# Kernel tuning notes

Hardware: AMD Instinct MI355X
Metric: run time of the kernel (lower is better)

Reference implementation:

```python
import jax, jax.numpy as jnp
import numpy as np

B, N, K = 8, 1024, 20


def _w(key, o, i):
    return jax.random.normal(key, (o, i), dtype=jnp.float32) * (1.0 / np.sqrt(i))


def setup_inputs() -> dict:
    key = jax.random.key(0)
    ks = iter(jax.random.split(key, 64))
    d = {"inputs": jax.random.normal(next(ks), (B, 3, N, 1), dtype=jnp.float32)}
    shapes = {
        "he_w1": (32, 12), "he_w2": (64, 32), "hn_w1": (32, 67), "hn_w2": (64, 32),
        "b1e_w1": (48, 192), "b1e_w2": (128, 48), "b1n_w1": (48, 192), "b1n_w2": (128, 48),
        "b2e_w1": (96, 384), "b2e_w2": (192, 96), "b2n_w1": (96, 320), "b2n_w2": (192, 96),
        "f_w": (512, 384), "p1_w": (256, 512), "p2_w": (128, 256), "p3_w": (40, 128),
    }
    for name, (o, i) in shapes.items():
        d[name] = _w(next(ks), o, i)
        d[name.replace("_w", "_b")] = jnp.zeros((o,), dtype=jnp.float32)
    return d


def _conv(x, w, b):
    # BasicConv with norm=None: 1x1 Conv2d + bias. x: [B,C,N,k]
    return jnp.einsum('bcnk,oc->bonk', x, w) + b[None, :, None, None]


def _conv_relu(x, w, b):
    return jax.nn.relu(_conv(x, w, b))


def _gather(x, idx):
    # batched_index_select: x [B,C,N,1], idx [B,N,k] -> [B,C,N,k]
    b, c, n, _ = x.shape
    k = idx.shape[-1]
    out = jnp.take_along_axis(x[:, :, :, 0], idx.reshape(b, 1, n * k), axis=2)
    return out.reshape(b, c, n, k)


def _knn(x, k):
    # DenseKnnGraph: x [B,C,N,1] -> (nn_idx, center_idx), each [B,N,k]
    xt = jnp.transpose(x[:, :, :, 0], (0, 2, 1))  # [B,N,C]
    sq = jnp.sum(xt * xt, axis=-1, keepdims=True)
    dist = sq - 2.0 * jnp.einsum('bnc,bmc->bnm', xt, xt) + jnp.transpose(sq, (0, 2, 1))
    _, nn_idx = jax.lax.top_k(-dist, k)
    center = jnp.broadcast_to(jnp.arange(x.shape[2])[None, :, None], nn_idx.shape)
    return nn_idx, center


def _mp(nf, e_ij, nn_idx, center, ew1, eb1, ew2, eb2, nw1, nb1, nw2, nb2):
    # MessagePassing block (Kearnes et al. style)
    h_i = _gather(nf, center)  # [B,Cin,N,k]
    h_j = _gather(nf, nn_idx)
    e_p = _conv_relu(_conv_relu(jnp.concatenate([e_ij, h_i, h_j], axis=1), ew1, eb1), ew2, eb2)
    m = jnp.broadcast_to(jnp.sum(e_p, axis=3, keepdims=True),
                         e_p.shape[:3] + (h_i.shape[-1],))
    h_p = _conv_relu(_conv_relu(jnp.concatenate([h_i, m], axis=1), nw1, nb1), nw2, nb2)
    return h_p[:, :, :, 0:1], e_p


def reference(inputs, he_w1, he_b1, he_w2, he_b2, hn_w1, hn_b1, hn_w2, hn_b2,
              b1e_w1, b1e_b1, b1e_w2, b1e_b2, b1n_w1, b1n_b1, b1n_w2, b1n_b2,
              b2e_w1, b2e_b1, b2e_w2, b2e_b2, b2n_w1, b2n_b1, b2n_w2, b2n_b2,
              f_w, f_b, p1_w, p1_b, p2_w, p2_b, p3_w, p3_b):
    nn_idx, center = _knn(inputs[:, 0:3], K)
    # initial edge features: (h_i, h_i - h_j) on xyz-KNN graph
    gh_i = _gather(inputs, center)
    gh_j = _gather(inputs, nn_idx)
    e_ij = jnp.concatenate([gh_i, gh_i - gh_j], axis=1)  # [B, 2*in, N, k]
    h1, e1 = _mp(inputs, e_ij, nn_idx, center, he_w1, he_b1, he_w2, he_b2, hn_w1, hn_b1, hn_w2, hn_b2)
    h2, e2 = _mp(h1, e1, nn_idx, center, b1e_w1, b1e_b1, b1e_w2, b1e_b2, b1n_w1, b1n_b1, b1n_w2, b1n_b2)
    h3, e3 = _mp(h2, e2, nn_idx, center, b2e_w1, b2e_b1, b2e_w2, b2e_b2, b2n_w1, b2n_b1, b2n_w2, b2n_b2)
    feats = jnp.concatenate([h1, h2, h3], axis=1)  # [B, 384, N, 1]
    fus = _conv_relu(feats, f_w, f_b)  # [B, 512, N, 1]
    pooled = jnp.max(fus, axis=(2, 3), keepdims=True)  # max_pool2d over [N,1]
    # prediction head (dropout = identity at inference)
    pred = _conv(_conv_relu(_conv_relu(pooled, p1_w, p1_b), p2_w, p2_b), p3_w, p3_b)
    return pred[:, :, :, 0], inputs  # (logits [B,n_classes,1], edge_features)
```

## Files before the change

kernel.cpp:

```cpp
#include <hip/hip_runtime.h>

#define BDIM 8
#define NDIM 1024
#define KNN 20

typedef unsigned short u16;
typedef float f32x4 __attribute__((ext_vector_type(4)));
typedef short short8 __attribute__((ext_vector_type(8)));
typedef unsigned short ushort8 __attribute__((ext_vector_type(8)));

__device__ inline u16 f2bf(float f) {
  unsigned u = __float_as_uint(f);
  unsigned r = (u + 0x7fffu + ((u >> 16) & 1u)) >> 16;
  return (u16)r;
}
__device__ inline float bf2f(u16 v) {
  return __uint_as_float(((unsigned)v) << 16);
}

__global__ __launch_bounds__(256) void knn_wcvt(
    const float* __restrict__ x, int* __restrict__ nn,
    const float* __restrict__ w1_3, const float* __restrict__ w2_3,
    const float* __restrict__ w1_2, const float* __restrict__ w2_2,
    const float* __restrict__ hn_w1, const float* __restrict__ f_w,
    const float* __restrict__ he_w1, const float* __restrict__ he_w2,
    const float* __restrict__ bn_w1, const float* __restrict__ bn_w2,
    u16* __restrict__ w1b3e, u16* __restrict__ wpq3, u16* __restrict__ w2b3,
    u16* __restrict__ w1b2e, u16* __restrict__ wpq2, u16* __restrict__ w2b2,
    float* __restrict__ w1p1, u16* __restrict__ fwb,
    u16* __restrict__ w1b1, u16* __restrict__ w2b1,
    u16* __restrict__ wn1b, u16* __restrict__ wn2b, int* __restrict__ pooled) {
  const int tid = threadIdx.x;
  if (blockIdx.x >= BDIM * 256) {
    const int idx = (blockIdx.x - BDIM * 256) * 256 + tid;
    if (idx < 512 * 384) fwb[idx] = f2bf(f_w[idx]);
    if (idx < 96 * 128) {
      int oc = idx >> 7, c = idx & 127;
      w1b3e[idx] = f2bf(w1_3[oc * 384 + c]);
    }
    if (idx < 192 * 128) {
      int n = idx >> 7, c = idx & 127;
      wpq3[idx] = f2bf(n < 96 ? w1_3[n * 384 + 128 + c]
                              : w1_3[(n - 96) * 384 + 256 + c]);
    }
    if (idx < 192 * 96) w2b3[idx] = f2bf(w2_3[idx]);
    if (idx < 48 * 64) {
      int oc = idx >> 6, c = idx & 63;
      w1b2e[idx] = f2bf(w1_2[oc * 192 + c]);
    }
    if (idx < 96 * 64) {
      int n = idx >> 6, c = idx & 63;
      wpq2[idx] = f2bf(n < 48 ? w1_2[n * 192 + 64 + c]
                              : w1_2[(n - 48) * 192 + 128 + c]);
    }
    if (idx < 128 * 64) {
      int oc = idx >> 6, i = idx & 63;
      w2b2[idx] = (i < 48) ? f2bf(w2_2[oc * 48 + i]) : (u16)0;
    }
    if (idx < 32 * 68) {
      int oc = idx / 68, c = idx - oc * 68;
      w1p1[idx] = (c < 67) ? hn_w1[oc * 67 + c] : 0.0f;
    }
    if (idx < 32 * 32) {
      int oc = idx >> 5, c = idx & 31;
      w1b1[idx] = (c < 12) ? f2bf(he_w1[oc * 12 + c]) : (u16)0;
    }
    if (idx < 64 * 32) w2b1[idx] = f2bf(he_w2[idx]);
    if (idx < 96 * 320) wn1b[idx] = f2bf(bn_w1[idx]);
    if (idx < 192 * 96) wn2b[idx] = f2bf(bn_w2[idx]);
    if (idx < BDIM * 512) pooled[idx] = 0;
    return;
  }
  {
#pragma clang fp contract(off)
    __shared__ float xs0[NDIM], xs1[NDIM], xs2[NDIM], sq[NDIM];
    const int lane = tid & 63;
    const int w = tid >> 6;
    const int b = blockIdx.x >> 8;
    const int n = ((blockIdx.x & 255) << 2) + w;
    for (int i = tid; i < NDIM; i += 256) {
      float a0 = x[(b * 3 + 0) * NDIM + i];
      float a1 = x[(b * 3 + 1) * NDIM + i];
      float a2 = x[(b * 3 + 2) * NDIM + i];
      xs0[i] = a0; xs1[i] = a1; xs2[i] = a2;
      sq[i] = (a0 * a0 + a1 * a1) + a2 * a2;
    }
    __syncthreads();
    const float xn0 = xs0[n], xn1 = xs1[n], xn2 = xs2[n], sqn = sq[n];
    float dl[16];
#pragma unroll
    for (int t = 0; t < 16; ++t) {
      int m = t * 64 + lane;
      float dot = (xn0 * xs0[m] + xn1 * xs1[m]) + xn2 * xs2[m];
      dl[t] = (sqn - 2.0f * dot) + sq[m];
    }
    int* nnrow = &nn[(b * NDIM + n) * KNN];
    for (int r = 0; r < KNN; ++r) {
      float bd = dl[0];
      int bt = 0;
#pragma unroll
      for (int t = 1; t < 16; ++t) {
        if (dl[t] < bd) { bd = dl[t]; bt = t; }
      }
      int bi = bt * 64 + lane;
#pragma unroll
      for (int off = 1; off < 64; off <<= 1) {
        float pd = __shfl_xor(bd, off);
        int pi = __shfl_xor(bi, off);
        if (pd < bd || (pd == bd && pi < bi)) { bd = pd; bi = pi; }
      }
      if (lane == 0) nnrow[r] = bi;
      if ((bi & 63) == lane) {
        int wt = bi >> 6;
#pragma unroll
        for (int t = 0; t < 16; ++t) {
          if (t == wt) dl[t] = 3.4e38f;
        }
      }
    }
  }
}

template <int PTS, int CE, int CMID, int COUT, bool WRITE_E, bool FIRST>
__global__ __launch_bounds__(256) void edge_mfma(
    const u16* __restrict__ eprev, const float* __restrict__ finput,
    const int* __restrict__ nnb, const u16* __restrict__ w1b,
    const float* __restrict__ b1v, const u16* __restrict__ w2b,
    const float* __restrict__ b2v, const u16* __restrict__ pq,
    u16* __restrict__ eout, float* __restrict__ mout) {
  constexpr int K2 = (CMID + 31) & ~31;
  constexpr int NPQ = 2 * CMID;
  constexpr int MT = PTS * KNN;
  constexpr int MTL = MT / 16;
  constexpr int XPB = CE + 8;
  constexpr int QYP = K2 + 8;
  __shared__ u16 Xs[MT * XPB];
  __shared__ u16 QY[MT * QYP];
  __shared__ float pld[FIRST ? 8 : PTS * CMID];
  const int tid = threadIdx.x;
  const int lane = tid & 63;
  const int wv = tid >> 6;
  const int q = lane >> 4;
  const int bn0 = blockIdx.x * PTS;
  const int b = bn0 >> 10;
  if constexpr (FIRST) {
    for (int idx = tid; idx < MT * (CE / 8); idx += 256) {
      int p = idx / (CE / 8), kc = idx - p * (CE / 8);
      int k0 = kc * 8;
      int bn = bn0 + p / KNN;
      int n = bn & (NDIM - 1);
      int j = nnb[(size_t)bn0 * KNN + p];
      ushort8 r;
#pragma unroll
      for (int t = 0; t < 8; ++t) {
        int c = k0 + t;
        float v = 0.0f;
        if (c < 3) v = finput[(b * 3 + c) * NDIM + n];
        else if (c < 6)
          v = finput[(b * 3 + c - 3) * NDIM + n] -
              finput[(b * 3 + c - 3) * NDIM + j];
        else if (c < 9) v = finput[(b * 3 + c - 6) * NDIM + n];
        else if (c < 12) v = finput[(b * 3 + c - 9) * NDIM + j];
        r[t] = f2bf(v);
      }
      *(ushort8*)&Xs[p * XPB + k0] = r;
    }
  } else {
    constexpr int KC = CE / 8;
    for (int ch = tid; ch < MT * KC; ch += 256) {
      int p = ch / KC, kc = ch - p * KC;
      int k0 = kc * 8;
      *(uint4*)&Xs[p * XPB + k0] =
          *(const uint4*)&eprev[((size_t)blockIdx.x * MT + p) * CE + k0];
    }
    constexpr int QC = CMID / 8;
    for (int i = tid; i < MT * QC; i += 256) {
      int p = i / QC, c8 = (i - p * QC) * 8;
      int j = nnb[(size_t)bn0 * KNN + p];
      *(uint4*)&QY[p * QYP + c8] =
          *(const uint4*)&pq[((size_t)(b << 10) + j) * NPQ + CMID + c8];
    }
    if constexpr (K2 != CMID) {
      constexpr int PC = (K2 - CMID) / 8;
      for (int i = tid; i < MT * PC; i += 256) {
        int p = i / PC, c8 = CMID + (i - p * PC) * 8;
        uint4 z = {0, 0, 0, 0};
        *(uint4*)&QY[p * QYP + c8] = z;
      }
    }
    for (int i = tid; i < PTS * CMID; i += 256) {
      int pt = i / CMID, c = i - pt * CMID;
      pld[i] = bf2f(pq[(size_t)(bn0 + pt) * NPQ + c]) + b1v[c];
    }
  }
  __syncthreads();
  {
    constexpr int NT1 = CMID / 16;
    constexpr int J1 = MTL * NT1;
    constexpr int KS1 = CE / 32;
    for (int job = wv; job < J1; job += 4) {
      int mt = job / NT1, nt = job - mt * NT1;
      int row = mt * 16 + (lane & 15);
      int ncol = nt * 16 + (lane & 15);
      int kb = q * 8;
      f32x4 acc = {0.f, 0.f, 0.f, 0.f};
      const u16* ap = &Xs[row * XPB + kb];
      const u16* bp = &w1b[(size_t)ncol * CE + kb];
#pragma unroll
      for (int ks = 0; ks < KS1; ++ks) {
        short8 a = *(const short8*)(ap + ks * 32);
        short8 bb = *(const short8*)(bp + ks * 32);
        acc = __builtin_amdgcn_mfma_f32_16x16x32_bf16(a, bb, acc, 0, 0, 0);
      }
      int m0 = mt * 16 + q * 4;
      if constexpr (FIRST) {
        float bias = b1v[ncol];
#pragma unroll
        for (int r = 0; r < 4; ++r) {
          float yv = fmaxf(acc[r] + bias, 0.0f);
          QY[(m0 + r) * QYP + ncol] = f2bf(yv);
        }
      } else {
        int pt = m0 / KNN;
        float padd = pld[pt * CMID + ncol];
#pragma unroll
        for (int r = 0; r < 4; ++r) {
          int m = m0 + r;
          float qadd = bf2f(QY[m * QYP + ncol]);
          float yv = fmaxf(acc[r] + padd + qadd, 0.0f);
          QY[m * QYP + ncol] = f2bf(yv);
        }
      }
    }
  }
  __syncthreads();
  {
    constexpr int NT2 = COUT / 16;
    constexpr int KS2 = K2 / 32;
    for (int nt = wv; nt < NT2; nt += 4) {
      int ncol = nt * 16 + (lane & 15);
      int kb = q * 8;
      short8 bfrag[KS2];
      const u16* bp = &w2b[(size_t)ncol * K2 + kb];
#pragma unroll
      for (int ks = 0; ks < KS2; ++ks)
        bfrag[ks] = *(const short8*)(bp + ks * 32);
      float bias = b2v[ncol];
      float s[PTS];
#pragma unroll
      for (int pt = 0; pt < PTS; ++pt) s[pt] = 0.0f;
#pragma unroll
      for (int mt = 0; mt < MTL; ++mt) {
        f32x4 acc = {0.f, 0.f, 0.f, 0.f};
        const u16* ap = &QY[(mt * 16 + (lane & 15)) * QYP + kb];
#pragma unroll
        for (int ks = 0; ks < KS2; ++ks) {
          short8 a = *(const short8*)(ap + ks * 32);
          acc = __builtin_amdgcn_mfma_f32_16x16x32_bf16(a, bfrag[ks], acc, 0, 0, 0);
        }
        int m0 = mt * 16 + q * 4;
        float part = 0.0f;
#pragma unroll
        for (int r = 0; r < 4; ++r) {
          float yv = fmaxf(acc[r] + bias, 0.0f);
          if (WRITE_E)
            eout[((size_t)blockIdx.x * MT + m0 + r) * COUT + ncol] = f2bf(yv);
          part += yv;
        }
        int ptA = (4 * mt) / 5;
        int ptB = (4 * mt + 3) / 5;
        int qb = 5 * ptB - 4 * mt;
#pragma unroll
        for (int pt2 = 0; pt2 < PTS; ++pt2) {
          if (pt2 == ptA && ptA == ptB) s[pt2] += part;
          else if (pt2 == ptA) s[pt2] += (q < qb) ? part : 0.0f;
          else if (pt2 == ptB) s[pt2] += (q < qb) ? 0.0f : part;
        }
      }
#pragma unroll
      for (int pt = 0; pt < PTS; ++pt) {
        float sv = s[pt];
        sv += __shfl_xor(sv, 16);
        sv += __shfl_xor(sv, 32);
        if (lane < 16)
          mout[(size_t)(bn0 + pt) * COUT + nt * 16 + lane] = sv;
      }
    }
  }
}

template <int TP, int CH, int CM, int CINP, int CMID, int COUT, int NPQ, bool FIRSTH>
__global__ __launch_bounds__(256) void node_conv(
    const float* __restrict__ h, const float* __restrict__ inputs,
    const float* __restrict__ mbuf, const float* __restrict__ w1p,
    const float* __restrict__ b1v, const float* __restrict__ w2,
    const float* __restrict__ b2v, float* __restrict__ hout,
    const u16* __restrict__ wpq, u16* __restrict__ pq) {
  constexpr int CIN = CH + CM;
  constexpr int XP = CINP + 4;
  constexpr int Y1P = CMID + 4;
  constexpr int PG = TP / 4;
  constexpr int HP = COUT + 8;
  __shared__ float Xs[TP * XP];
  __shared__ float Y1s[TP * Y1P];
  __shared__ u16 Hb[(NPQ > 0) ? TP * HP : 8];
  const int tid = threadIdx.x;
  const int bn0 = blockIdx.x * TP;
  if constexpr (FIRSTH) {
    for (int idx = tid; idx < TP * CIN; idx += 256) {
      int p = idx / CIN, c = idx - p * CIN;
      int bn = bn0 + p;
      int b = bn >> 10, n = bn & (NDIM - 1);
      Xs[p * XP + c] = (c < CH) ? inputs[(b * 3 + c) * NDIM + n]
                                : mbuf[(size_t)bn * CM + (c - CH)];
    }
    if constexpr (CINP > CIN) {
      constexpr int PAD = CINP - CIN;
      for (int idx = tid; idx < TP * PAD; idx += 256) {
        int p = idx / PAD, c = CIN + idx % PAD;
        Xs[p * XP + c] = 0.0f;
      }
    }
  } else {
    constexpr int C4 = CIN / 4;
    for (int idx = tid; idx < TP * C4; idx += 256) {
      int p = idx / C4, c = (idx - p * C4) * 4;
      int bn = bn0 + p;
      float4 v = (c < CH) ? *(const float4*)&h[(size_t)bn * CH + c]
                          : *(const float4*)&mbuf[(size_t)bn * CM + (c - CH)];
      *(float4*)&Xs[p * XP + c] = v;
    }
  }
  __syncthreads();
  {
    constexpr int NT1 = PG * (CMID / 4);
    for (int t = tid; t < NT1; t += 256) {
      int pg = t % PG, og = t / PG;
      float acc[4][4];
#pragma unroll
      for (int j = 0; j < 4; ++j) {
        float bj = b1v[og * 4 + j];
#pragma unroll
        for (int i = 0; i < 4; ++i) acc[i][j] = bj;
      }
      for (int cin = 0; cin < CINP; cin += 4) {
        float4 xr[4], wr[4];
#pragma unroll
        for (int i = 0; i < 4; ++i)
          xr[i] = *(const float4*)&Xs[(pg * 4 + i) * XP + cin];
#pragma unroll
        for (int j = 0; j < 4; ++j)
          wr[j] = *(const float4*)&w1p[(size_t)(og * 4 + j) * CINP + cin];
#pragma unroll
        for (int i = 0; i < 4; ++i)
#pragma unroll
          for (int j = 0; j < 4; ++j) {
            acc[i][j] += xr[i].x * wr[j].x;
            acc[i][j] += xr[i].y * wr[j].y;
            acc[i][j] += xr[i].z * wr[j].z;
            acc[i][j] += xr[i].w * wr[j].w;
          }
      }
#pragma unroll
      for (int i = 0; i < 4; ++i)
#pragma unroll
        for (int j = 0; j < 4; ++j)
          Y1s[(pg * 4 + i) * Y1P + og * 4 + j] = fmaxf(acc[i][j], 0.0f);
    }
  }
  __syncthreads();
  {
    constexpr int NT2 = PG * (COUT / 4);
    for (int t = tid; t < NT2; t += 256) {
      int pg = t % PG, og = t / PG;
      float acc[4][4];
#pragma unroll
      for (int j = 0; j < 4; ++j) {
        float bj = b2v[og * 4 + j];
#pragma unroll
        for (int i = 0; i < 4; ++i) acc[i][j] = bj;
      }
      for (int cin = 0; cin < CMID; cin += 4) {
        float4 xr[4], wr[4];
#pragma unroll
        for (int i = 0; i < 4; ++i)
          xr[i] = *(const float4*)&Y1s[(pg * 4 + i) * Y1P + cin];
#pragma unroll
        for (int j = 0; j < 4; ++j)
          wr[j] = *(const float4*)&w2[(size_t)(og * 4 + j) * CMID + cin];
#pragma unroll
        for (int i = 0; i < 4; ++i)
#pragma unroll
          for (int j = 0; j < 4; ++j) {
            acc[i][j] += xr[i].x * wr[j].x;
            acc[i][j] += xr[i].y * wr[j].y;
            acc[i][j] += xr[i].z * wr[j].z;
            acc[i][j] += xr[i].w * wr[j].w;
          }
      }
#pragma unroll
      for (int i = 0; i < 4; ++i) {
        int bn = bn0 + pg * 4 + i;
#pragma unroll
        for (int j = 0; j < 4; ++j) {
          float v = fmaxf(acc[i][j], 0.0f);
          hout[(size_t)bn * COUT + og * 4 + j] = v;
          if constexpr (NPQ > 0) Hb[(pg * 4 + i) * HP + og * 4 + j] = f2bf(v);
        }
      }
    }
  }
  if constexpr (NPQ > 0) {
    __syncthreads();
    const int lane = tid & 63;
    const int wv = tid >> 6;
    constexpr int NT = NPQ / 16;
    constexpr int JOBS = (TP / 16) * NT;
    constexpr int KS = COUT / 32;
    for (int job = wv; job < JOBS; job += 4) {
      int mt = job / NT, nt = job - mt * NT;
      int row = mt * 16 + (lane & 15);
      int ncol = nt * 16 + (lane & 15);
      int kb = (lane >> 4) * 8;
      f32x4 acc = {0.f, 0.f, 0.f, 0.f};
      const u16* ap = &Hb[row * HP + kb];
      const u16* bp = &wpq[(size_t)ncol * COUT + kb];
#pragma unroll
      for (int ks = 0; ks < KS; ++ks) {
        short8 a = *(const short8*)(ap + ks * 32);
        short8 bb = *(const short8*)(bp + ks * 32);
        acc = __builtin_amdgcn_mfma_f32_16x16x32_bf16(a, bb, acc, 0, 0, 0);
      }
      int m0 = mt * 16 + (lane >> 4) * 4;
#pragma unroll
      for (int r = 0; r < 4; ++r)
        pq[(size_t)(bn0 + m0 + r) * NPQ + ncol] = f2bf(acc[r]);
    }
  }
}

__global__ __launch_bounds__(256) void fuse_pool_mfma(
    const float* __restrict__ h1, const float* __restrict__ h2,
    const float* __restrict__ m3, const u16* __restrict__ wn1b,
    const float* __restrict__ bn1v, const u16* __restrict__ wn2b,
    const float* __restrict__ bn2v, const u16* __restrict__ fwb,
    const float* __restrict__ fb, int* __restrict__ pooled) {
  constexpr int TP = 32;
  constexpr int XNP = 328;
  constexpr int Y1NP = 104;
  constexpr int XPB = 392;
  __shared__ __align__(16) char smem[TP * XPB * 2];
  u16* Xs = (u16*)smem;
  u16* Xn = (u16*)smem;
  __shared__ u16 Y1n[TP * Y1NP];
  __shared__ int pmax[512];
  const int tid = threadIdx.x;
  const int lane = tid & 63;
  const int wv = tid >> 6;
  const int q = lane >> 4;
  const int bn0 = blockIdx.x * TP;
  const int b = bn0 >> 10;
  for (int i = tid; i < 512; i += 256) pmax[i] = 0;
  for (int i = tid; i < TP * 41; i += 256) {
    int p = i / 41, kc = i - p * 41;
    int k0 = kc * 8;
    ushort8 r;
    if (kc < 16) {
      const float* src = &h2[(size_t)(bn0 + p) * 128 + k0];
      float4 f0 = *(const float4*)src;
      float4 f1 = *(const float4*)(src + 4);
      r[0] = f2bf(f0.x); r[1] = f2bf(f0.y); r[2] = f2bf(f0.z); r[3] = f2bf(f0.w);
      r[4] = f2bf(f1.x); r[5] = f2bf(f1.y); r[6] = f2bf(f1.z); r[7] = f2bf(f1.w);
    } else if (kc < 40) {
      const float* src = &m3[(size_t)(bn0 + p) * 192 + (k0 - 128)];
      float4 f0 = *(const float4*)src;
      float4 f1 = *(const float4*)(src + 4);
      r[0] = f2bf(f0.x); r[1] = f2bf(f0.y); r[2] = f2bf(f0.z); r[3] = f2bf(f0.w);
      r[4] = f2bf(f1.x); r[5] = f2bf(f1.y); r[6] = f2bf(f1.z); r[7] = f2bf(f1.w);
    } else {
#pragma unroll
      for (int t = 0; t < 8; ++t) r[t] = 0;
    }
    *(ushort8*)&Xn[p * XNP + k0] = r;
  }
  __syncthreads();
  for (int job = wv; job < 12; job += 4) {
    int mt = job / 6, nt = job - mt * 6;
    int row = mt * 16 + (lane & 15);
    int ncol = nt * 16 + (lane & 15);
    int kb = q * 8;
    f32x4 acc = {0.f, 0.f, 0.f, 0.f};
    const u16* ap = &Xn[row * XNP + kb];
    const u16* bp = &wn1b[(size_t)ncol * 320 + kb];
#pragma unroll
    for (int ks = 0; ks < 10; ++ks) {
      short8 a = *(const short8*)(ap + ks * 32);
      short8 bb = *(const short8*)(bp + ks * 32);
      acc = __builtin_amdgcn_mfma_f32_16x16x32_bf16(a, bb, acc, 0, 0, 0);
    }
    float bias = bn1v[ncol];
    int m0 = mt * 16 + q * 4;
#pragma unroll
    for (int r = 0; r < 4; ++r)
      Y1n[(m0 + r) * Y1NP + ncol] = f2bf(fmaxf(acc[r] + bias, 0.0f));
  }
  __syncthreads();
  for (int i = tid; i < TP * 24; i += 256) {
    int p = i / 24, kc = i - p * 24;
    int k0 = kc * 8;
    const float* src = (k0 < 64) ? &h1[(size_t)(bn0 + p) * 64 + k0]
                                 : &h2[(size_t)(bn0 + p) * 128 + (k0 - 64)];
    float4 f0 = *(const float4*)src;
    float4 f1 = *(const float4*)(src + 4);
    ushort8 r;
    r[0] = f2bf(f0.x); r[1] = f2bf(f0.y); r[2] = f2bf(f0.z); r[3] = f2bf(f0.w);
    r[4] = f2bf(f1.x); r[5] = f2bf(f1.y); r[6] = f2bf(f1.z); r[7] = f2bf(f1.w);
    *(ushort8*)&Xs[p * XPB + k0] = r;
  }
  if (tid < TP) {
    ushort8 z = {0, 0, 0, 0, 0, 0, 0, 0};
    *(ushort8*)&Xs[tid * XPB + 384] = z;
  }
  for (int job = wv; job < 24; job += 4) {
    int mt = job / 12, nt = job - mt * 12;
    int row = mt * 16 + (lane & 15);
    int ncol = nt * 16 + (lane & 15);
    int kb = q * 8;
    f32x4 acc = {0.f, 0.f, 0.f, 0.f};
    const u16* ap = &Y1n[row * Y1NP + kb];
    const u16* bp = &wn2b[(size_t)ncol * 96 + kb];
#pragma unroll
    for (int ks = 0; ks < 3; ++ks) {
      short8 a = *(const short8*)(ap + ks * 32);
      short8 bb = *(const short8*)(bp + ks * 32);
      acc = __builtin_amdgcn_mfma_f32_16x16x32_bf16(a, bb, acc, 0, 0, 0);
    }
    float bias = bn2v[ncol];
    int m0 = mt * 16 + q * 4;
#pragma unroll
    for (int r = 0; r < 4; ++r)
      Xs[(m0 + r) * XPB + 192 + ncol] = f2bf(fmaxf(acc[r] + bias, 0.0f));
  }
  __syncthreads();
  for (int job = wv; job < 64; job += 4) {
    int mt = job / 32, nt = job - mt * 32;
    int row = mt * 16 + (lane & 15);
    int ncol = nt * 16 + (lane & 15);
    int kb = q * 8;
    f32x4 acc = {0.f, 0.f, 0.f, 0.f};
    const u16* ap = &Xs[row * XPB + kb];
    const u16* bp = &fwb[(size_t)ncol * 384 + kb];
#pragma unroll
    for (int ks = 0; ks < 12; ++ks) {
      short8 a = *(const short8*)(ap + ks * 32);
      short8 bb = *(const short8*)(bp + ks * 32);
      acc = __builtin_amdgcn_mfma_f32_16x16x32_bf16(a, bb, acc, 0, 0, 0);
    }
    float bias = fb[ncol];
    float v = fmaxf(fmaxf(acc[0], acc[1]), fmaxf(acc[2], acc[3]));
    v = fmaxf(v + bias, 0.0f);
    v = fmaxf(v, __shfl_xor(v, 16));
    v = fmaxf(v, __shfl_xor(v, 32));
    if (lane < 16) atomicMax(&pmax[ncol], __float_as_int(v));
  }
  __syncthreads();
  for (int i = tid; i < 512; i += 256)
    atomicMax(&pooled[b * 512 + i], pmax[i]);
}

__global__ __launch_bounds__(256) void head_kernel(
    const int* __restrict__ pooledi, const float* __restrict__ p1w,
    const float* __restrict__ p1b, const float* __restrict__ p2w,
    const float* __restrict__ p2b, const float* __restrict__ p3w,
    const float* __restrict__ p3b, const float* __restrict__ inputs,
    float* __restrict__ out) {
  const int tid = threadIdx.x;
  if (blockIdx.x >= BDIM) {
    int idx = (blockIdx.x - BDIM) * 256 + tid;
    if (idx < (BDIM * 3 * NDIM) / 4) {
      const float4* src = (const float4*)inputs;
      float4* dst = (float4*)(out + BDIM * 40);
      dst[idx] = src[idx];
    }
    return;
  }
  __shared__ float xs[512], y1[256], y2[128];
  const int b = blockIdx.x;
  for (int i = tid; i < 512; i += 256) xs[i] = __int_as_float(pooledi[b * 512 + i]);
  __syncthreads();
  {
    float acc = p1b[tid];
    for (int c = 0; c < 512; ++c) acc += xs[c] * p1w[tid * 512 + c];
    y1[tid] = fmaxf(acc, 0.0f);
  }
  __syncthreads();
  if (tid < 128) {
    float acc = p2b[tid];
    for (int c = 0; c < 256; ++c) acc += y1[c] * p2w[tid * 256 + c];
    y2[tid] = fmaxf(acc, 0.0f);
  }
  __syncthreads();
  if (tid < 40) {
    float acc = p3b[tid];
    for (int c = 0; c < 128; ++c) acc += y2[c] * p3w[tid * 128 + c];
    out[b * 40 + tid] = acc;
  }
}

extern "C" void kernel_launch(void* const* d_in, const int* in_sizes, int n_in,
                              void* d_out, int out_size, void* d_ws,
                              size_t ws_size, hipStream_t stream) {
  const float* inputs = (const float*)d_in[0];
  const float* he_w1 = (const float*)d_in[1];
  const float* he_b1 = (const float*)d_in[2];
  const float* he_w2 = (const float*)d_in[3];
  const float* he_b2 = (const float*)d_in[4];
  const float* hn_w1 = (const float*)d_in[5];
  const float* hn_b1 = (const float*)d_in[6];
  const float* hn_w2 = (const float*)d_in[7];
  const float* hn_b2 = (const float*)d_in[8];
  const float* b1e_w1 = (const float*)d_in[9];
  const float* b1e_b1 = (const float*)d_in[10];
  const float* b1e_w2 = (const float*)d_in[11];
  const float* b1e_b2 = (const float*)d_in[12];
  const float* b1n_w1 = (const float*)d_in[13];
  const float* b1n_b1 = (const float*)d_in[14];
  const float* b1n_w2 = (const float*)d_in[15];
  const float* b1n_b2 = (const float*)d_in[16];
  const float* b2e_w1 = (const float*)d_in[17];
  const float* b2e_b1 = (const float*)d_in[18];
  const float* b2e_w2 = (const float*)d_in[19];
  const float* b2e_b2 = (const float*)d_in[20];
  const float* b2n_w1 = (const float*)d_in[21];
  const float* b2n_b1 = (const float*)d_in[22];
  const float* b2n_w2 = (const float*)d_in[23];
  const float* b2n_b2 = (const float*)d_in[24];
  const float* f_w = (const float*)d_in[25];
  const float* f_b = (const float*)d_in[26];
  const float* p1_w = (const float*)d_in[27];
  const float* p1_b = (const float*)d_in[28];
  const float* p2_w = (const float*)d_in[29];
  const float* p2_b = (const float*)d_in[30];
  const float* p3_w = (const float*)d_in[31];
  const float* p3_b = (const float*)d_in[32];
  float* out = (float*)d_out;

  char* ws = (char*)d_ws;
  size_t off = 0;
  auto alloc = [&](size_t bytes) {
    void* p = ws + off;
    off += (bytes + 255) & ~(size_t)255;
    return p;
  };
  int* nn = (int*)alloc((size_t)BDIM * NDIM * KNN * 4);
  float* m1 = (float*)alloc((size_t)BDIM * NDIM * 64 * 4);
  float* h1 = (float*)alloc((size_t)BDIM * NDIM * 64 * 4);
  u16* e1 = (u16*)alloc((size_t)BDIM * NDIM * KNN * 64 * 2);
  float* m2 = (float*)alloc((size_t)BDIM * NDIM * 128 * 4);
  float* h2 = (float*)alloc((size_t)BDIM * NDIM * 128 * 4);
  u16* e2 = (u16*)alloc((size_t)BDIM * NDIM * KNN * 128 * 2);
  float* m3 = (float*)alloc((size_t)BDIM * NDIM * 192 * 4);
  u16* pq2 = (u16*)alloc((size_t)BDIM * NDIM * 96 * 2);
  u16* pq3 = (u16*)alloc((size_t)BDIM * NDIM * 192 * 2);
  int* pooled = (int*)alloc((size_t)BDIM * 512 * 4);
  u16* w1b3e = (u16*)alloc((size_t)96 * 128 * 2);
  u16* wpq3 = (u16*)alloc((size_t)192 * 128 * 2);
  u16* w2b3 = (u16*)alloc((size_t)192 * 96 * 2);
  u16* w1b2e = (u16*)alloc((size_t)48 * 64 * 2);
  u16* wpq2 = (u16*)alloc((size_t)96 * 64 * 2);
  u16* w2b2 = (u16*)alloc((size_t)128 * 64 * 2);
  float* w1p1 = (float*)alloc((size_t)32 * 68 * 4);
  u16* fwb = (u16*)alloc((size_t)512 * 384 * 2);
  u16* w1b1 = (u16*)alloc((size_t)32 * 32 * 2);
  u16* w2b1 = (u16*)alloc((size_t)64 * 32 * 2);
  u16* wn1b = (u16*)alloc((size_t)96 * 320 * 2);
  u16* wn2b = (u16*)alloc((size_t)192 * 96 * 2);

  knn_wcvt<<<BDIM * 256 + 768, 256, 0, stream>>>(
      inputs, nn, b2e_w1, b2e_w2, b1e_w1, b1e_w2, hn_w1, f_w, he_w1, he_w2,
      b2n_w1, b2n_w2, w1b3e, wpq3, w2b3, w1b2e, wpq2, w2b2, w1p1, fwb, w1b1,
      w2b1, wn1b, wn2b, pooled);

  edge_mfma<4, 32, 32, 64, true, true><<<BDIM * NDIM / 4, 256, 0, stream>>>(
      nullptr, inputs, nn, w1b1, he_b1, w2b1, he_b2, nullptr, e1, m1);
  node_conv<64, 3, 64, 68, 32, 64, 96, true><<<BDIM * NDIM / 64, 256, 0, stream>>>(
      nullptr, inputs, m1, w1p1, hn_b1, hn_w2, hn_b2, h1, wpq2, pq2);

  edge_mfma<4, 64, 48, 128, true, false><<<BDIM * NDIM / 4, 256, 0, stream>>>(
      e1, nullptr, nn, w1b2e, b1e_b1, w2b2, b1e_b2, pq2, e2, m2);
  node_conv<32, 64, 128, 192, 48, 128, 192, false><<<BDIM * NDIM / 32, 256, 0, stream>>>(
      h1, nullptr, m2, b1n_w1, b1n_b1, b1n_w2, b1n_b2, h2, wpq3, pq3);

  edge_mfma<4, 128, 96, 192, false, false><<<BDIM * NDIM / 4, 256, 0, stream>>>(
      e2, nullptr, nn, w1b3e, b2e_b1, w2b3, b2e_b2, pq3, nullptr, m3);

  fuse_pool_mfma<<<BDIM * NDIM / 32, 256, 0, stream>>>(
      h1, h2, m3, wn1b, b2n_b1, wn2b, b2n_b2, fwb, f_b, pooled);
  head_kernel<<<BDIM + 24, 256, 0, stream>>>(pooled, p1_w, p1_b, p2_w, p2_b,
                                             p3_w, p3_b, inputs, out);
}
```

Before: 225.2 us.

## Replace second node conv with bf16 MFMA kernel and widen knn blocks

Adds a dedicated node2_mfma kernel that computes the block-1 node MLP (192->48->128) and the following pq projection with bf16 MFMA tiles held in shared memory, replacing the generic fp32 node_conv instantiation. Weights for this stage are converted to bf16 (the second layer zero-padded to K=64) inside the existing knn/weight-conversion kernel. Separately, the knn kernel moves to 512-thread blocks, each handling 8 query points instead of 4, so the per-batch coordinates are loaded into shared memory half as often. The MFMA path lowers precision of the node features and h2 to bf16 inputs, which may shift numerics slightly.

```diff
diff --git a/kernel.cpp b/kernel.cpp
--- a/kernel.cpp
+++ b/kernel.cpp
@@ -18,21 +18,24 @@
   return __uint_as_float(((unsigned)v) << 16);
 }
 
-__global__ __launch_bounds__(256) void knn_wcvt(
+__global__ __launch_bounds__(512) void knn_wcvt(
     const float* __restrict__ x, int* __restrict__ nn,
     const float* __restrict__ w1_3, const float* __restrict__ w2_3,
     const float* __restrict__ w1_2, const float* __restrict__ w2_2,
     const float* __restrict__ hn_w1, const float* __restrict__ f_w,
     const float* __restrict__ he_w1, const float* __restrict__ he_w2,
     const float* __restrict__ bn_w1, const float* __restrict__ bn_w2,
+    const float* __restrict__ n2_w1, const float* __restrict__ n2_w2,
     u16* __restrict__ w1b3e, u16* __restrict__ wpq3, u16* __restrict__ w2b3,
     u16* __restrict__ w1b2e, u16* __restrict__ wpq2, u16* __restrict__ w2b2,
     float* __restrict__ w1p1, u16* __restrict__ fwb,
     u16* __restrict__ w1b1, u16* __restrict__ w2b1,
-    u16* __restrict__ wn1b, u16* __restrict__ wn2b, int* __restrict__ pooled) {
+    u16* __restrict__ wn1b, u16* __restrict__ wn2b,
+    u16* __restrict__ wn21b, u16* __restrict__ wn22b,
+    int* __restrict__ pooled) {
   const int tid = threadIdx.x;
-  if (blockIdx.x >= BDIM * 256) {
-    const int idx = (blockIdx.x - BDIM * 256) * 256 + tid;
+  if (blockIdx.x >= BDIM * 128) {
+    const int idx = (blockIdx.x - BDIM * 128) * 512 + tid;
     if (idx < 512 * 384) fwb[idx] = f2bf(f_w[idx]);
     if (idx < 96 * 128) {
       int oc = idx >> 7, c = idx & 127;
@@ -68,6 +71,11 @@
     if (idx < 64 * 32) w2b1[idx] = f2bf(he_w2[idx]);
     if (idx < 96 * 320) wn1b[idx] = f2bf(bn_w1[idx]);
     if (idx < 192 * 96) wn2b[idx] = f2bf(bn_w2[idx]);
+    if (idx < 48 * 192) wn21b[idx] = f2bf(n2_w1[idx]);
+    if (idx < 128 * 64) {
+      int oc = idx >> 6, i = idx & 63;
+      wn22b[idx] = (i < 48) ? f2bf(n2_w2[oc * 48 + i]) : (u16)0;
+    }
     if (idx < BDIM * 512) pooled[idx] = 0;
     return;
   }
@@ -76,9 +84,9 @@
     __shared__ float xs0[NDIM], xs1[NDIM], xs2[NDIM], sq[NDIM];
     const int lane = tid & 63;
     const int w = tid >> 6;
-    const int b = blockIdx.x >> 8;
-    const int n = ((blockIdx.x & 255) << 2) + w;
-    for (int i = tid; i < NDIM; i += 256) {
+    const int b = blockIdx.x >> 7;
+    const int n = ((blockIdx.x & 127) << 3) + w;
+    for (int i = tid; i < NDIM; i += 512) {
       float a0 = x[(b * 3 + 0) * NDIM + i];
       float a1 = x[(b * 3 + 1) * NDIM + i];
       float a2 = x[(b * 3 + 2) * NDIM + i];
@@ -436,6 +444,105 @@
       for (int r = 0; r < 4; ++r)
         pq[(size_t)(bn0 + m0 + r) * NPQ + ncol] = f2bf(acc[r]);
     }
+  }
+}
+
+__global__ __launch_bounds__(256) void node2_mfma(
+    const float* __restrict__ h1, const float* __restrict__ m2,
+    const u16* __restrict__ w1b, const float* __restrict__ b1v,
+    const u16* __restrict__ w2b, const float* __restrict__ b2v,
+    float* __restrict__ h2out, const u16* __restrict__ wpq,
+    u16* __restrict__ pq) {
+  constexpr int TP = 32, XP = 200, Y1P = 72, HP = 136;
+  __shared__ u16 Xb[TP * XP];
+  __shared__ u16 Y1[TP * Y1P];
+  __shared__ u16 Hb[TP * HP];
+  const int tid = threadIdx.x;
+  const int lane = tid & 63;
+  const int wv = tid >> 6;
+  const int q = lane >> 4;
+  const int bn0 = blockIdx.x * TP;
+  for (int i = tid; i < TP * 24; i += 256) {
+    int p = i / 24, kc = i - p * 24;
+    int k0 = kc * 8;
+    const float* src = (k0 < 64) ? &h1[(size_t)(bn0 + p) * 64 + k0]
+                                 : &m2[(size_t)(bn0 + p) * 128 + (k0 - 64)];
+    float4 f0 = *(const float4*)src;
+    float4 f1 = *(const float4*)(src + 4);
+    ushort8 r;
+    r[0] = f2bf(f0.x); r[1] = f2bf(f0.y); r[2] = f2bf(f0.z); r[3] = f2bf(f0.w);
+    r[4] = f2bf(f1.x); r[5] = f2bf(f1.y); r[6] = f2bf(f1.z); r[7] = f2bf(f1.w);
+    *(ushort8*)&Xb[p * XP + k0] = r;
+  }
+  for (int i = tid; i < TP * 2; i += 256) {
+    int p = i >> 1, c8 = 48 + (i & 1) * 8;
+    ushort8 z = {0, 0, 0, 0, 0, 0, 0, 0};
+    *(ushort8*)&Y1[p * Y1P + c8] = z;
+  }
+  __syncthreads();
+  for (int job = wv; job < 6; job += 4) {
+    int mt = job / 3, nt = job - mt * 3;
+    int row = mt * 16 + (lane & 15);
+    int ncol = nt * 16 + (lane & 15);
+    int kb = q * 8;
+    f32x4 acc = {0.f, 0.f, 0.f, 0.f};
+    const u16* ap = &Xb[row * XP + kb];
+    const u16* bp = &w1b[(size_t)ncol * 192 + kb];
+#pragma unroll
+    for (int ks = 0; ks < 6; ++ks) {
+      short8 a = *(const short8*)(ap + ks * 32);
+      short8 bb = *(const short8*)(bp + ks * 32);
+      acc = __builtin_amdgcn_mfma_f32_16x16x32_bf16(a, bb, acc, 0, 0, 0);
+    }
+    float bias = b1v[ncol];
+    int m0 = mt * 16 + q * 4;
+#pragma unroll
+    for (int r = 0; r < 4; ++r)
+      Y1[(m0 + r) * Y1P + ncol] = f2bf(fmaxf(acc[r] + bias, 0.0f));
+  }
+  __syncthreads();
+  for (int job = wv; job < 16; job += 4) {
+    int mt = job / 8, nt = job - mt * 8;
+    int row = mt * 16 + (lane & 15);
+    int ncol = nt * 16 + (lane & 15);
+    int kb = q * 8;
+    f32x4 acc = {0.f, 0.f, 0.f, 0.f};
+    const u16* ap = &Y1[row * Y1P + kb];
+    const u16* bp = &w2b[(size_t)ncol * 64 + kb];
+#pragma unroll
+    for (int ks = 0; ks < 2; ++ks) {
+      short8 a = *(const short8*)(ap + ks * 32);
+      short8 bb = *(const short8*)(bp + ks * 32);
+      acc = __builtin_amdgcn_mfma_f32_16x16x32_bf16(a, bb, acc, 0, 0, 0);
+    }
+    float bias = b2v[ncol];
+    int m0 = mt * 16 + q * 4;
+#pragma unroll
+    for (int r = 0; r < 4; ++r) {
+      float v = fmaxf(acc[r] + bias, 0.0f);
+      h2out[(size_t)(bn0 + m0 + r) * 128 + ncol] = v;
+      Hb[(m0 + r) * HP + ncol] = f2bf(v);
+    }
+  }
+  __syncthreads();
+  for (int job = wv; job < 24; job += 4) {
+    int mt = job / 12, nt = job - mt * 12;
+    int row = mt * 16 + (lane & 15);
+    int ncol = nt * 16 + (lane & 15);
+    int kb = q * 8;
+    f32x4 acc = {0.f, 0.f, 0.f, 0.f};
+    const u16* ap = &Hb[row * HP + kb];
+    const u16* bp = &wpq[(size_t)ncol * 128 + kb];
+#pragma unroll
+    for (int ks = 0; ks < 4; ++ks) {
+      short8 a = *(const short8*)(ap + ks * 32);
+      short8 bb = *(const short8*)(bp + ks * 32);
+      acc = __builtin_amdgcn_mfma_f32_16x16x32_bf16(a, bb, acc, 0, 0, 0);
+    }
+    int m0 = mt * 16 + q * 4;
+#pragma unroll
+    for (int r = 0; r < 4; ++r)
+      pq[(size_t)(bn0 + m0 + r) * 192 + ncol] = f2bf(acc[r]);
   }
 }
 
@@ -675,11 +782,13 @@
   u16* w2b1 = (u16*)alloc((size_t)64 * 32 * 2);
   u16* wn1b = (u16*)alloc((size_t)96 * 320 * 2);
   u16* wn2b = (u16*)alloc((size_t)192 * 96 * 2);
-
-  knn_wcvt<<<BDIM * 256 + 768, 256, 0, stream>>>(
+  u16* wn21b = (u16*)alloc((size_t)48 * 192 * 2);
+  u16* wn22b = (u16*)alloc((size_t)128 * 64 * 2);
+
+  knn_wcvt<<<BDIM * 128 + 384, 512, 0, stream>>>(
       inputs, nn, b2e_w1, b2e_w2, b1e_w1, b1e_w2, hn_w1, f_w, he_w1, he_w2,
-      b2n_w1, b2n_w2, w1b3e, wpq3, w2b3, w1b2e, wpq2, w2b2, w1p1, fwb, w1b1,
-      w2b1, wn1b, wn2b, pooled);
+      b2n_w1, b2n_w2, b1n_w1, b1n_w2, w1b3e, wpq3, w2b3, w1b2e, wpq2, w2b2,
+      w1p1, fwb, w1b1, w2b1, wn1b, wn2b, wn21b, wn22b, pooled);
 
   edge_mfma<4, 32, 32, 64, true, true><<<BDIM * NDIM / 4, 256, 0, stream>>>(
       nullptr, inputs, nn, w1b1, he_b1, w2b1, he_b2, nullptr, e1, m1);
@@ -688,8 +797,8 @@
 
   edge_mfma<4, 64, 48, 128, true, false><<<BDIM * NDIM / 4, 256, 0, stream>>>(
       e1, nullptr, nn, w1b2e, b1e_b1, w2b2, b1e_b2, pq2, e2, m2);
-  node_conv<32, 64, 128, 192, 48, 128, 192, false><<<BDIM * NDIM / 32, 256, 0, stream>>>(
-      h1, nullptr, m2, b1n_w1, b1n_b1, b1n_w2, b1n_b2, h2, wpq3, pq3);
+  node2_mfma<<<BDIM * NDIM / 32, 256, 0, stream>>>(
+      h1, m2, wn21b, b1n_b1, wn22b, b1n_b2, h2, wpq3, pq3);
 
   edge_mfma<4, 128, 96, 192, false, false><<<BDIM * NDIM / 4, 256, 0, stream>>>(
       e2, nullptr, nn, w1b3e, b2e_b1, w2b3, b2e_b2, pq3, nullptr, m3);
```

Result: faster. 214.5 us, median of 2 (-4.7%).
